# Kernel optimization log

Hardware: AMD Instinct MI355X
Metric: run time of the kernel (lower is better)

Reference implementation:

```python
import jax, jax.numpy as jnp
import numpy as np

B, S, E = 4, 2048, 1024


def setup_inputs() -> dict:
    key = jax.random.key(0)
    k1, k2, k3, k4 = jax.random.split(key, 4)
    scale = 1.0 / np.sqrt(E)
    return {
        "x": jax.random.normal(k1, (B, S, E), dtype=jnp.float32),
        "W_Q": jax.random.normal(k2, (E, E), dtype=jnp.float32) * scale,
        "W_K": jax.random.normal(k3, (E, E), dtype=jnp.float32) * scale,
        "W_V": jax.random.normal(k4, (E, E), dtype=jnp.float32) * scale,
    }


def reference(x, W_Q, W_K, W_V):
    # nn.Linear(E, E, bias=False): y = x @ W.T
    Q = jnp.einsum("bse,fe->bsf", x, W_Q)
    K = jnp.einsum("bse,fe->bsf", x, W_K)
    V = jnp.einsum("bse,fe->bsf", x, W_V)
    d = Q.shape[-1]
    scores = jnp.einsum("bqd,bkd->bqk", Q, K) / jnp.sqrt(jnp.float32(d))
    # causal mask: -inf strictly above the diagonal
    seq = Q.shape[1]
    causal = jnp.tril(jnp.ones((seq, seq), dtype=bool))  # [S,S]
    scores = jnp.where(causal[None, :, :], scores, jnp.float32(-jnp.inf))
    attn = jax.nn.softmax(scores, axis=-1)
    return jnp.einsum("bqk,bkd->bqd", attn, V)
```

## Files before the change

### kernel.cpp

```cpp
#include <hip/hip_runtime.h>
#include <hip/hip_bf16.h>
#include <stdint.h>

typedef __hip_bfloat16 bf16;
typedef __attribute__((ext_vector_type(8))) short bf16x8;
typedef __attribute__((ext_vector_type(4))) float f32x4;
typedef __attribute__((ext_vector_type(8))) unsigned short u16x8;
typedef __attribute__((ext_vector_type(4))) unsigned short u16x4;

#define SLEN 2048
#define ED   1024
#define NB   4
#define AS1 __attribute__((address_space(1)))
#define AS3 __attribute__((address_space(3)))

static __device__ __forceinline__ unsigned short f2bf(float f) {
    return __builtin_bit_cast(unsigned short, __float2bfloat16(f));
}

__device__ __forceinline__ void gemm2p(
    const char* __restrict__ aT, int lda,
    const char* __restrict__ bT, int ldb,
    int nkt, char* sm, int tid, f32x4 (&acc)[4][4])
{
    const int lane = tid & 63, wave = tid >> 6;
    const int wm = wave >> 1, wn = wave & 1;
    const int fr = lane & 15, kc = lane >> 4;

    auto STAGE = [&](int kh, int Tn) {
        char* base = sm + (Tn & 1) * 32768 + kh * 8192;
#pragma unroll
        for (int half = 0; half < 2; ++half) {
            const char* g = half ? bT : aT;
            const int ld = half ? ldb : lda;
            char* pb = base + half * 16384;
#pragma unroll
            for (int j = 0; j < 2; ++j) {
                int rid = j * 256 + tid;
                int row = rid >> 2, c = rid & 3;
                const char* src = g + (size_t)row * ld + Tn * 128 + kh * 64
                                + ((c ^ ((row >> 1) & 3)) * 16);
                __builtin_amdgcn_global_load_lds(
                    (const AS1 uint32_t*)src,
                    (AS3 uint32_t*)(pb + (j * 256 + wave * 64) * 16),
                    16, 0, 0);
            }
        }
    };

    STAGE(0, 0); STAGE(1, 0);
    asm volatile("s_waitcnt vmcnt(4)" ::: "memory");
    __builtin_amdgcn_sched_barrier(0);
    __builtin_amdgcn_s_barrier();

    for (int T = 0; T < nkt; ++T) {
        const bool pre = (T + 1 < nkt);
#pragma unroll
        for (int kh = 0; kh < 2; ++kh) {
            const char* buf = sm + (T & 1) * 32768 + kh * 8192;
            bf16x8 a[4], b[4];
#pragma unroll
            for (int i = 0; i < 4; ++i) {
                int row = wm * 64 + i * 16 + fr;
                a[i] = *(const bf16x8*)(buf + row * 64 + ((kc ^ ((row >> 1) & 3)) * 16));
            }
#pragma unroll
            for (int i = 0; i < 4; ++i) {
                int row = wn * 64 + i * 16 + fr;
                b[i] = *(const bf16x8*)(buf + 16384 + row * 64 + ((kc ^ ((row >> 1) & 3)) * 16));
            }
            if (pre) {
                STAGE(kh, T + 1);
                asm volatile("s_waitcnt vmcnt(4)" ::: "memory");
            } else {
                asm volatile("s_waitcnt vmcnt(0)" ::: "memory");
            }
            __builtin_amdgcn_sched_barrier(0);
            __builtin_amdgcn_s_barrier();
            asm volatile("s_waitcnt lgkmcnt(0)" ::: "memory");
            __builtin_amdgcn_sched_barrier(0);
            __builtin_amdgcn_s_setprio(1);
#pragma unroll
            for (int i = 0; i < 4; ++i)
#pragma unroll
                for (int n = 0; n < 4; ++n)
                    acc[i][n] = __builtin_amdgcn_mfma_f32_16x16x32_bf16(
                        a[i], b[n], acc[i][n], 0, 0, 0);
            __builtin_amdgcn_s_setprio(0);
        }
    }
}

__global__ __launch_bounds__(256) void convert_to_bf16(
    const float* __restrict__ x, const float* __restrict__ wq,
    const float* __restrict__ wk, const float* __restrict__ wv,
    bf16* __restrict__ xb, bf16* __restrict__ wqb,
    bf16* __restrict__ wkb, bf16* __restrict__ wvb)
{
    long g = (long)blockIdx.x * 256 + threadIdx.x;
    const float* src; bf16* dst; long o;
    if (g < 1048576) { src = x; dst = xb; o = g * 8; }
    else {
        long g2 = g - 1048576;
        int w = (int)(g2 >> 17);
        o = (g2 & 131071) * 8;
        src = (w == 0) ? wq : (w == 1) ? wk : wv;
        dst = (w == 0) ? wqb : (w == 1) ? wkb : wvb;
    }
    float4 v0 = *(const float4*)(src + o);
    float4 v1 = *(const float4*)(src + o + 4);
    u16x8 r;
    r[0] = f2bf(v0.x); r[1] = f2bf(v0.y); r[2] = f2bf(v0.z); r[3] = f2bf(v0.w);
    r[4] = f2bf(v1.x); r[5] = f2bf(v1.y); r[6] = f2bf(v1.z); r[7] = f2bf(v1.w);
    *(u16x8*)(dst + o) = r;
}

__global__ __launch_bounds__(256, 2) void qkv_gemm(
    const bf16* __restrict__ xb, const bf16* __restrict__ wqb,
    const bf16* __restrict__ wkb, const bf16* __restrict__ wvb,
    bf16* __restrict__ Qb, bf16* __restrict__ Kb, bf16* __restrict__ Vt)
{
    extern __shared__ char smem[];
    int bid = blockIdx.x, tid = threadIdx.x;
    int xcd = bid & 7, i = bid >> 3;
    int tm = (xcd << 3) | (i & 7);
    int tn = i >> 3;
    const bf16* W = (tn < 8) ? wqb : (tn < 16) ? wkb : wvb;
    int tnl = tn & 7;
    f32x4 acc[4][4] = {};
    gemm2p((const char*)(xb + (size_t)tm * 128 * ED), ED * 2,
           (const char*)(W + (size_t)tnl * 128 * ED), ED * 2,
           16, smem, tid, acc);

    int lane = tid & 63, wave = tid >> 6, wm = wave >> 1, wn = wave & 1;
    int rl = (lane >> 4) * 4, cl = lane & 15;
    if (tn < 16) {
        bf16* C = (tn < 8) ? Qb : Kb;
#pragma unroll
        for (int mf = 0; mf < 4; ++mf)
#pragma unroll
            for (int j = 0; j < 4; ++j) {
                int r = tm * 128 + wm * 64 + mf * 16 + rl + j;
#pragma unroll
                for (int nf = 0; nf < 4; ++nf) {
                    int c = tnl * 128 + wn * 64 + nf * 16 + cl;
                    C[(size_t)r * ED + c] = __float2bfloat16(acc[mf][nf][j]);
                }
            }
    } else {
#pragma unroll
        for (int mf = 0; mf < 4; ++mf)
#pragma unroll
            for (int j = 0; j < 4; ++j) {
                int r = tm * 128 + wm * 64 + mf * 16 + rl + j;
                int bb = r >> 11, s = r & 2047;
#pragma unroll
                for (int nf = 0; nf < 4; ++nf) {
                    int d = tnl * 128 + wn * 64 + nf * 16 + cl;
                    Vt[(((size_t)bb << 10) + d) * SLEN + s] = __float2bfloat16(acc[mf][nf][j]);
                }
            }
    }
}

__global__ __launch_bounds__(256, 2) void qk_gemm(
    const bf16* __restrict__ Qb, const bf16* __restrict__ Kb, float* __restrict__ Sc)
{
    extern __shared__ char smem[];
    int bx = blockIdx.x, b = blockIdx.y, tid = threadIdx.x;
    int t = (bx & 7) * 17 + (bx >> 3);
    int ti = 0;
    while ((ti + 1) * (ti + 2) / 2 <= t) ++ti;
    int tj = t - ti * (ti + 1) / 2;
    f32x4 acc[4][4] = {};
    gemm2p((const char*)(Qb + ((size_t)b * SLEN + ti * 128) * ED), ED * 2,
           (const char*)(Kb + ((size_t)b * SLEN + tj * 128) * ED), ED * 2,
           16, smem, tid, acc);

    float* Sb = Sc + (size_t)b * SLEN * SLEN;
    int lane = tid & 63, wave = tid >> 6, wm = wave >> 1, wn = wave & 1;
    int rl = (lane >> 4) * 4, cl = lane & 15;
#pragma unroll
    for (int mf = 0; mf < 4; ++mf)
#pragma unroll
        for (int j = 0; j < 4; ++j) {
            int r = ti * 128 + wm * 64 + mf * 16 + rl + j;
#pragma unroll
            for (int nf = 0; nf < 4; ++nf) {
                int c = tj * 128 + wn * 64 + nf * 16 + cl;
                Sb[(size_t)r * SLEN + c] = acc[mf][nf][j] * 0.03125f;
            }
        }
}

__global__ __launch_bounds__(256) void softmax_rows(float* __restrict__ Sc)
{
    int q = blockIdx.x, b = blockIdx.y, tid = threadIdx.x;
    float* row = Sc + ((size_t)b * SLEN + q) * SLEN;
    int lane = tid & 63, wave = tid >> 6;
    __shared__ float red[4];

    float vals[8];
    float lmax = -3.0e38f;
#pragma unroll
    for (int r = 0; r < 2; ++r) {
        int i4 = tid + r * 256;
        float4 v = *(const float4*)(row + i4 * 4);
        vals[r * 4 + 0] = v.x; vals[r * 4 + 1] = v.y;
        vals[r * 4 + 2] = v.z; vals[r * 4 + 3] = v.w;
#pragma unroll
        for (int e = 0; e < 4; ++e) {
            int k = i4 * 4 + e;
            if (k <= q) lmax = fmaxf(lmax, vals[r * 4 + e]);
        }
    }
#pragma unroll
    for (int o = 32; o > 0; o >>= 1) lmax = fmaxf(lmax, __shfl_xor(lmax, o));
    if (lane == 0) red[wave] = lmax;
    __syncthreads();
    float m = fmaxf(fmaxf(red[0], red[1]), fmaxf(red[2], red[3]));
    __syncthreads();
    float lsum = 0.f;
#pragma unroll
    for (int r = 0; r < 2; ++r)
#pragma unroll
        for (int e = 0; e < 4; ++e) {
            int k = (tid + r * 256) * 4 + e;
            if (k <= q) lsum += __expf(vals[r * 4 + e] - m);
        }
#pragma unroll
    for (int o = 32; o > 0; o >>= 1) lsum += __shfl_xor(lsum, o);
    if (lane == 0) red[wave] = lsum;
    __syncthreads();
    float inv = 1.0f / (red[0] + red[1] + red[2] + red[3]);
    unsigned short* prow = (unsigned short*)row;
#pragma unroll
    for (int r = 0; r < 2; ++r) {
        int i4 = tid + r * 256;
        u16x4 o4;
#pragma unroll
        for (int e = 0; e < 4; ++e) {
            int k = i4 * 4 + e;
            float p = (k <= q) ? __expf(vals[r * 4 + e] - m) * inv : 0.0f;
            o4[e] = f2bf(p);
        }
        *(u16x4*)(prow + i4 * 4) = o4;
    }
}

__global__ __launch_bounds__(256, 2) void pv_gemm(
    const bf16* __restrict__ P, const bf16* __restrict__ Vt, float* __restrict__ O)
{
    extern __shared__ char smem[];
    int mq = 15 - blockIdx.x, nd = blockIdx.y, b = blockIdx.z, tid = threadIdx.x;
    f32x4 acc[4][4] = {};
    int nkt = (mq + 1) * 2;
    gemm2p((const char*)P + ((size_t)b * SLEN + mq * 128) * 8192, 8192,
           (const char*)(Vt + ((size_t)b * ED + nd * 128) * SLEN), SLEN * 2,
           nkt, smem, tid, acc);

    int lane = tid & 63, wave = tid >> 6, wm = wave >> 1, wn = wave & 1;
    int rl = (lane >> 4) * 4, cl = lane & 15;
    float* Ob = O + (size_t)b * SLEN * ED;
#pragma unroll
    for (int mf = 0; mf < 4; ++mf)
#pragma unroll
        for (int j = 0; j < 4; ++j) {
            int r = mq * 128 + wm * 64 + mf * 16 + rl + j;
#pragma unroll
            for (int nf = 0; nf < 4; ++nf) {
                int c = nd * 128 + wn * 64 + nf * 16 + cl;
                Ob[(size_t)r * ED + c] = acc[mf][nf][j];
            }
        }
}

extern "C" void kernel_launch(void* const* d_in, const int* in_sizes, int n_in,
                              void* d_out, int out_size, void* d_ws, size_t ws_size,
                              hipStream_t stream)
{
    const float* x  = (const float*)d_in[0];
    const float* wq = (const float*)d_in[1];
    const float* wk = (const float*)d_in[2];
    const float* wv = (const float*)d_in[3];
    float* out = (float*)d_out;

    char* ws = (char*)d_ws;
    bf16* xb  = (bf16*)(ws);
    bf16* wqb = (bf16*)(ws + 16777216);
    bf16* wkb = (bf16*)(ws + 18874368);
    bf16* wvb = (bf16*)(ws + 20971520);
    bf16* Qb  = (bf16*)(ws + 23068672);
    bf16* Kb  = (bf16*)(ws + 39845888);
    bf16* Vt  = (bf16*)(ws + 56623104);
    float* Sc = (float*)(ws + 73400320);

    (void)hipFuncSetAttribute((const void*)qkv_gemm,
            hipFuncAttributeMaxDynamicSharedMemorySize, 65536);
    (void)hipFuncSetAttribute((const void*)qk_gemm,
            hipFuncAttributeMaxDynamicSharedMemorySize, 65536);
    (void)hipFuncSetAttribute((const void*)pv_gemm,
            hipFuncAttributeMaxDynamicSharedMemorySize, 65536);

    convert_to_bf16<<<5632, 256, 0, stream>>>(x, wq, wk, wv, xb, wqb, wkb, wvb);
    qkv_gemm<<<1536, 256, 65536, stream>>>(xb, wqb, wkb, wvb, Qb, Kb, Vt);
    qk_gemm<<<dim3(136, NB), 256, 65536, stream>>>(Qb, Kb, Sc);
    softmax_rows<<<dim3(SLEN, NB), 256, 0, stream>>>(Sc);
    pv_gemm<<<dim3(16, 8, NB), 256, 65536, stream>>>((const bf16*)Sc, Vt, out);
}
```

Baseline: 164.3 us.

## Enlarge GEMM tiles to 256x128 with 512-thread blocks; skip masked softmax loads

The shared GEMM core now computes 256x128 output tiles using 8 waves per block and a 96KB double-buffered LDS layout. This halves the block count and doubles reuse of the B operand, with an extra barrier per k-half to protect the buffers. The QKV, QK and PV kernels are remapped to the larger M tiles, including a new triangular tile enumeration for 256x128 causal blocks. Softmax now skips global loads and arithmetic for masked-out column groups. The trade-offs are lower occupancy per CU, since two 96KB blocks may not fit in LDS at once, and coarser load balancing for the triangular PV work.

```diff
diff --git a/kernel.cpp b/kernel.cpp
--- a/kernel.cpp
+++ b/kernel.cpp
@@ -18,7 +18,7 @@
     return __builtin_bit_cast(unsigned short, __float2bfloat16(f));
 }
 
-__device__ __forceinline__ void gemm2p(
+__device__ __forceinline__ void gemm_core(
     const char* __restrict__ aT, int lda,
     const char* __restrict__ bT, int ldb,
     int nkt, char* sm, int tid, f32x4 (&acc)[4][4])
@@ -28,50 +28,55 @@
     const int fr = lane & 15, kc = lane >> 4;
 
     auto STAGE = [&](int kh, int Tn) {
-        char* base = sm + (Tn & 1) * 32768 + kh * 8192;
-#pragma unroll
-        for (int half = 0; half < 2; ++half) {
-            const char* g = half ? bT : aT;
-            const int ld = half ? ldb : lda;
-            char* pb = base + half * 16384;
-#pragma unroll
-            for (int j = 0; j < 2; ++j) {
-                int rid = j * 256 + tid;
-                int row = rid >> 2, c = rid & 3;
-                const char* src = g + (size_t)row * ld + Tn * 128 + kh * 64
-                                + ((c ^ ((row >> 1) & 3)) * 16);
-                __builtin_amdgcn_global_load_lds(
-                    (const AS1 uint32_t*)src,
-                    (AS3 uint32_t*)(pb + (j * 256 + wave * 64) * 16),
-                    16, 0, 0);
-            }
+        char* buf = sm + (Tn & 1) * 49152;
+#pragma unroll
+        for (int j = 0; j < 2; ++j) {
+            int rid = j * 512 + tid;
+            int row = rid >> 2, c = rid & 3;
+            const char* src = aT + (size_t)row * lda + Tn * 128 + kh * 64
+                            + ((c ^ ((row >> 1) & 3)) * 16);
+            __builtin_amdgcn_global_load_lds(
+                (const AS1 uint32_t*)src,
+                (AS3 uint32_t*)(buf + kh * 16384 + (j * 512 + wave * 64) * 16),
+                16, 0, 0);
+        }
+        {
+            int row = tid >> 2, c = tid & 3;
+            const char* src = bT + (size_t)row * ldb + Tn * 128 + kh * 64
+                            + ((c ^ ((row >> 1) & 3)) * 16);
+            __builtin_amdgcn_global_load_lds(
+                (const AS1 uint32_t*)src,
+                (AS3 uint32_t*)(buf + 32768 + kh * 8192 + (wave * 64) * 16),
+                16, 0, 0);
         }
     };
 
     STAGE(0, 0); STAGE(1, 0);
-    asm volatile("s_waitcnt vmcnt(4)" ::: "memory");
+    asm volatile("s_waitcnt vmcnt(3)" ::: "memory");
     __builtin_amdgcn_sched_barrier(0);
     __builtin_amdgcn_s_barrier();
 
     for (int T = 0; T < nkt; ++T) {
         const bool pre = (T + 1 < nkt);
+        const char* buf = sm + (T & 1) * 49152;
 #pragma unroll
         for (int kh = 0; kh < 2; ++kh) {
-            const char* buf = sm + (T & 1) * 32768 + kh * 8192;
             bf16x8 a[4], b[4];
 #pragma unroll
             for (int i = 0; i < 4; ++i) {
                 int row = wm * 64 + i * 16 + fr;
-                a[i] = *(const bf16x8*)(buf + row * 64 + ((kc ^ ((row >> 1) & 3)) * 16));
+                a[i] = *(const bf16x8*)(buf + kh * 16384 + row * 64
+                                        + ((kc ^ ((row >> 1) & 3)) * 16));
             }
 #pragma unroll
             for (int i = 0; i < 4; ++i) {
                 int row = wn * 64 + i * 16 + fr;
-                b[i] = *(const bf16x8*)(buf + 16384 + row * 64 + ((kc ^ ((row >> 1) & 3)) * 16));
+                b[i] = *(const bf16x8*)(buf + 32768 + kh * 8192 + row * 64
+                                        + ((kc ^ ((row >> 1) & 3)) * 16));
             }
             if (pre) {
                 STAGE(kh, T + 1);
-                asm volatile("s_waitcnt vmcnt(4)" ::: "memory");
+                asm volatile("s_waitcnt vmcnt(3)" ::: "memory");
             } else {
                 asm volatile("s_waitcnt vmcnt(0)" ::: "memory");
             }
@@ -87,6 +92,7 @@
                     acc[i][n] = __builtin_amdgcn_mfma_f32_16x16x32_bf16(
                         a[i], b[n], acc[i][n], 0, 0, 0);
             __builtin_amdgcn_s_setprio(0);
+            __builtin_amdgcn_s_barrier();
         }
     }
 }
@@ -115,7 +121,7 @@
     *(u16x8*)(dst + o) = r;
 }
 
-__global__ __launch_bounds__(256, 2) void qkv_gemm(
+__global__ __launch_bounds__(512, 2) void qkv_gemm(
     const bf16* __restrict__ xb, const bf16* __restrict__ wqb,
     const bf16* __restrict__ wkb, const bf16* __restrict__ wvb,
     bf16* __restrict__ Qb, bf16* __restrict__ Kb, bf16* __restrict__ Vt)
@@ -123,14 +129,14 @@
     extern __shared__ char smem[];
     int bid = blockIdx.x, tid = threadIdx.x;
     int xcd = bid & 7, i = bid >> 3;
-    int tm = (xcd << 3) | (i & 7);
-    int tn = i >> 3;
+    int tm = (xcd << 2) | (i & 3);
+    int tn = i >> 2;
     const bf16* W = (tn < 8) ? wqb : (tn < 16) ? wkb : wvb;
     int tnl = tn & 7;
     f32x4 acc[4][4] = {};
-    gemm2p((const char*)(xb + (size_t)tm * 128 * ED), ED * 2,
-           (const char*)(W + (size_t)tnl * 128 * ED), ED * 2,
-           16, smem, tid, acc);
+    gemm_core((const char*)(xb + (size_t)tm * 256 * ED), ED * 2,
+              (const char*)(W + (size_t)tnl * 128 * ED), ED * 2,
+              16, smem, tid, acc);
 
     int lane = tid & 63, wave = tid >> 6, wm = wave >> 1, wn = wave & 1;
     int rl = (lane >> 4) * 4, cl = lane & 15;
@@ -140,7 +146,7 @@
         for (int mf = 0; mf < 4; ++mf)
 #pragma unroll
             for (int j = 0; j < 4; ++j) {
-                int r = tm * 128 + wm * 64 + mf * 16 + rl + j;
+                int r = tm * 256 + wm * 64 + mf * 16 + rl + j;
 #pragma unroll
                 for (int nf = 0; nf < 4; ++nf) {
                     int c = tnl * 128 + wn * 64 + nf * 16 + cl;
@@ -152,7 +158,7 @@
         for (int mf = 0; mf < 4; ++mf)
 #pragma unroll
             for (int j = 0; j < 4; ++j) {
-                int r = tm * 128 + wm * 64 + mf * 16 + rl + j;
+                int r = tm * 256 + wm * 64 + mf * 16 + rl + j;
                 int bb = r >> 11, s = r & 2047;
 #pragma unroll
                 for (int nf = 0; nf < 4; ++nf) {
@@ -163,19 +169,19 @@
     }
 }
 
-__global__ __launch_bounds__(256, 2) void qk_gemm(
+__global__ __launch_bounds__(512, 2) void qk_gemm(
     const bf16* __restrict__ Qb, const bf16* __restrict__ Kb, float* __restrict__ Sc)
 {
     extern __shared__ char smem[];
     int bx = blockIdx.x, b = blockIdx.y, tid = threadIdx.x;
-    int t = (bx & 7) * 17 + (bx >> 3);
+    int t = (bx & 7) * 9 + (bx >> 3);
     int ti = 0;
-    while ((ti + 1) * (ti + 2) / 2 <= t) ++ti;
-    int tj = t - ti * (ti + 1) / 2;
+    while ((ti + 1) * (ti + 2) <= t) ++ti;
+    int tj = t - ti * (ti + 1);
     f32x4 acc[4][4] = {};
-    gemm2p((const char*)(Qb + ((size_t)b * SLEN + ti * 128) * ED), ED * 2,
-           (const char*)(Kb + ((size_t)b * SLEN + tj * 128) * ED), ED * 2,
-           16, smem, tid, acc);
+    gemm_core((const char*)(Qb + ((size_t)b * SLEN + ti * 256) * ED), ED * 2,
+              (const char*)(Kb + ((size_t)b * SLEN + tj * 128) * ED), ED * 2,
+              16, smem, tid, acc);
 
     float* Sb = Sc + (size_t)b * SLEN * SLEN;
     int lane = tid & 63, wave = tid >> 6, wm = wave >> 1, wn = wave & 1;
@@ -184,7 +190,7 @@
     for (int mf = 0; mf < 4; ++mf)
 #pragma unroll
         for (int j = 0; j < 4; ++j) {
-            int r = ti * 128 + wm * 64 + mf * 16 + rl + j;
+            int r = ti * 256 + wm * 64 + mf * 16 + rl + j;
 #pragma unroll
             for (int nf = 0; nf < 4; ++nf) {
                 int c = tj * 128 + wn * 64 + nf * 16 + cl;
@@ -205,13 +211,15 @@
 #pragma unroll
     for (int r = 0; r < 2; ++r) {
         int i4 = tid + r * 256;
-        float4 v = *(const float4*)(row + i4 * 4);
-        vals[r * 4 + 0] = v.x; vals[r * 4 + 1] = v.y;
-        vals[r * 4 + 2] = v.z; vals[r * 4 + 3] = v.w;
-#pragma unroll
-        for (int e = 0; e < 4; ++e) {
-            int k = i4 * 4 + e;
-            if (k <= q) lmax = fmaxf(lmax, vals[r * 4 + e]);
+        if (i4 * 4 <= q) {
+            float4 v = *(const float4*)(row + i4 * 4);
+            vals[r * 4 + 0] = v.x; vals[r * 4 + 1] = v.y;
+            vals[r * 4 + 2] = v.z; vals[r * 4 + 3] = v.w;
+#pragma unroll
+            for (int e = 0; e < 4; ++e) {
+                int k = i4 * 4 + e;
+                if (k <= q) lmax = fmaxf(lmax, vals[r * 4 + e]);
+            }
         }
     }
 #pragma unroll
@@ -222,12 +230,15 @@
     __syncthreads();
     float lsum = 0.f;
 #pragma unroll
-    for (int r = 0; r < 2; ++r)
-#pragma unroll
-        for (int e = 0; e < 4; ++e) {
-            int k = (tid + r * 256) * 4 + e;
-            if (k <= q) lsum += __expf(vals[r * 4 + e] - m);
-        }
+    for (int r = 0; r < 2; ++r) {
+        int i4 = tid + r * 256;
+        if (i4 * 4 <= q)
+#pragma unroll
+            for (int e = 0; e < 4; ++e) {
+                int k = i4 * 4 + e;
+                if (k <= q) lsum += __expf(vals[r * 4 + e] - m);
+            }
+    }
 #pragma unroll
     for (int o = 32; o > 0; o >>= 1) lsum += __shfl_xor(lsum, o);
     if (lane == 0) red[wave] = lsum;
@@ -248,16 +259,16 @@
     }
 }
 
-__global__ __launch_bounds__(256, 2) void pv_gemm(
+__global__ __launch_bounds__(512, 2) void pv_gemm(
     const bf16* __restrict__ P, const bf16* __restrict__ Vt, float* __restrict__ O)
 {
     extern __shared__ char smem[];
-    int mq = 15 - blockIdx.x, nd = blockIdx.y, b = blockIdx.z, tid = threadIdx.x;
+    int mq = 7 - blockIdx.x, nd = blockIdx.y, b = blockIdx.z, tid = threadIdx.x;
     f32x4 acc[4][4] = {};
-    int nkt = (mq + 1) * 2;
-    gemm2p((const char*)P + ((size_t)b * SLEN + mq * 128) * 8192, 8192,
-           (const char*)(Vt + ((size_t)b * ED + nd * 128) * SLEN), SLEN * 2,
-           nkt, smem, tid, acc);
+    int nkt = (mq + 1) * 4;
+    gemm_core((const char*)P + ((size_t)b * SLEN + mq * 256) * 8192, 8192,
+              (const char*)(Vt + ((size_t)b * ED + nd * 128) * SLEN), SLEN * 2,
+              nkt, smem, tid, acc);
 
     int lane = tid & 63, wave = tid >> 6, wm = wave >> 1, wn = wave & 1;
     int rl = (lane >> 4) * 4, cl = lane & 15;
@@ -266,7 +277,7 @@
     for (int mf = 0; mf < 4; ++mf)
 #pragma unroll
         for (int j = 0; j < 4; ++j) {
-            int r = mq * 128 + wm * 64 + mf * 16 + rl + j;
+            int r = mq * 256 + wm * 64 + mf * 16 + rl + j;
 #pragma unroll
             for (int nf = 0; nf < 4; ++nf) {
                 int c = nd * 128 + wn * 64 + nf * 16 + cl;
@@ -296,15 +307,15 @@
     float* Sc = (float*)(ws + 73400320);
 
     (void)hipFuncSetAttribute((const void*)qkv_gemm,
-            hipFuncAttributeMaxDynamicSharedMemorySize, 65536);
+            hipFuncAttributeMaxDynamicSharedMemorySize, 98304);
     (void)hipFuncSetAttribute((const void*)qk_gemm,
-            hipFuncAttributeMaxDynamicSharedMemorySize, 65536);
+            hipFuncAttributeMaxDynamicSharedMemorySize, 98304);
     (void)hipFuncSetAttribute((const void*)pv_gemm,
-            hipFuncAttributeMaxDynamicSharedMemorySize, 65536);
+            hipFuncAttributeMaxDynamicSharedMemorySize, 98304);
 
     convert_to_bf16<<<5632, 256, 0, stream>>>(x, wq, wk, wv, xb, wqb, wkb, wvb);
-    qkv_gemm<<<1536, 256, 65536, stream>>>(xb, wqb, wkb, wvb, Qb, Kb, Vt);
-    qk_gemm<<<dim3(136, NB), 256, 65536, stream>>>(Qb, Kb, Sc);
+    qkv_gemm<<<768, 512, 98304, stream>>>(xb, wqb, wkb, wvb, Qb, Kb, Vt);
+    qk_gemm<<<dim3(72, NB), 512, 98304, stream>>>(Qb, Kb, Sc);
     softmax_rows<<<dim3(SLEN, NB), 256, 0, stream>>>(Sc);
-    pv_gemm<<<dim3(16, 8, NB), 256, 65536, stream>>>((const bf16*)Sc, Vt, out);
-}
+    pv_gemm<<<dim3(8, 8, NB), 512, 98304, stream>>>((const bf16*)Sc, Vt, out);
+}
```

After: 168.6 us. 1.03x slower.
